# Optimization experiments

Hardware: AMD Instinct MI355X
Metric: run time of the kernel (lower is better)

The kernel has to match this reference:

```python
import jax, jax.numpy as jnp
import numpy as np

HEADS, DIM_HEAD, INNER, DIM = 6, 50, 300, 768
HW, EXTRA, POOL = 100, 150, 10  # spatial side, extra tokens, pool output side
N = HW * HW + EXTRA  # 10150


def setup_inputs() -> dict:
    key = jax.random.key(0)
    ks = jax.random.split(key, 6)
    B = 8
    x = jax.random.normal(ks[0], (B, N, DIM), dtype=jnp.float32)
    # weights scaled ~ typical init so softmax logits are sane
    proj_w = jax.random.normal(ks[1], (INNER, DIM), dtype=jnp.float32) * 0.02
    step_x = jax.random.normal(ks[2], (HEADS, 1, 1), dtype=jnp.float32)
    step_rep = jax.random.normal(ks[3], (HEADS, 1, 1), dtype=jnp.float32)
    out_w = jax.random.normal(ks[4], (DIM, INNER), dtype=jnp.float32) * 0.02
    out_b = jax.random.normal(ks[5], (DIM,), dtype=jnp.float32) * 0.02
    return {"x": x, "proj_w": proj_w, "step_x": step_x, "step_rep": step_rep,
            "out_w": out_w, "out_b": out_b}


def reference(x, proj_w, step_x, step_rep, out_w, out_b):
    b, n, c = x.shape
    hw = int(round((n - EXTRA) ** 0.5))
    scale = DIM_HEAD ** -0.5

    w = x @ proj_w.T  # [b, n, 300]

    # adaptive avg pool of the spatial tokens to (10,10); hw % 10 == 0 -> uniform pooling
    k = hw // POOL
    spatial = w[:, : hw * hw, :].reshape(b, hw, hw, INNER).transpose(0, 3, 1, 2)  # [b,300,hw,hw]
    rep = spatial.reshape(b, INNER, POOL, k, POOL, k).mean(axis=(3, 5))  # [b,300,10,10]
    rep = rep.reshape(b, INNER, POOL * POOL).transpose(0, 2, 1)  # [b,100,300]

    wh = w.reshape(b, n, HEADS, DIM_HEAD).transpose(0, 2, 1, 3)        # [b,h,n,d]
    reph = rep.reshape(b, POOL * POOL, HEADS, DIM_HEAD).transpose(0, 2, 1, 3)  # [b,h,100,d]

    # stage 1: rep attends to all tokens
    dots = jnp.einsum('bhqd,bhkd->bhqk', reph, wh) * scale  # [b,h,100,n]
    attn = jax.nn.softmax(dots, axis=-1)
    rep_delta = jnp.einsum('bhqk,bhkd->bhqd', attn, wh)     # [b,h,100,d]
    reph = reph + step_rep * rep_delta

    # stage 2: rep self-attention, broadcast back through reused attn^T
    dots2 = jnp.einsum('bhqd,bhkd->bhqk', reph, reph) * scale  # [b,h,100,100]
    attn2 = jax.nn.softmax(dots2, axis=-1)
    x_delta = jnp.einsum('bhqk,bhkd->bhqd', attn2, reph)       # [b,h,100,d]
    x_delta = jnp.einsum('bhqn,bhqd->bhnd', attn, x_delta)     # attn^T @ x_delta -> [b,h,n,d]
    x_delta = step_x * x_delta

    x_delta = x_delta.transpose(0, 2, 1, 3).reshape(b, n, HEADS * DIM_HEAD)  # [b,n,300]
    return x_delta @ out_w.T + out_b
```

## Files before the change

kernel.cpp:

```cpp
#include <hip/hip_runtime.h>
#include <math.h>

#define BATCH   8
#define NTOK    10150
#define DIMC    768
#define INNERC  300
#define HEADS   6
#define DHEAD   50
#define NQ      100
#define NBH     48
#define NSPLIT  32
#define CHUNK   320
#define SCALE   0.14142135623730951f
#define MTOT    (BATCH*NTOK)
#define XDK     320
#define NEGBIG  -1.0e30f

typedef __attribute__((ext_vector_type(8))) short short8;
typedef __attribute__((ext_vector_type(4))) float f32x4;

__device__ __forceinline__ ushort f2bf(float x) {
  uint u = __float_as_uint(x);
  uint r = (u + 0x7fffu + ((u >> 16) & 1u)) >> 16;
  return (ushort)r;
}
__device__ __forceinline__ float bf2f(ushort h) {
  return __uint_as_float(((uint)h) << 16);
}

__global__ void split_pad(const float* __restrict__ src, ushort* __restrict__ dHi,
                          ushort* __restrict__ dLo, int R, int C, int Rp, int Cp) {
  const int total = Rp * Cp;
  for (int i = blockIdx.x * blockDim.x + threadIdx.x; i < total;
       i += gridDim.x * blockDim.x) {
    const int r = i / Cp, c = i % Cp;
    const float v = (r < R && c < C) ? src[r * C + c] : 0.f;
    const ushort hh = f2bf(v);
    dHi[i] = hh;
    dLo[i] = f2bf(v - bf2f(hh));
  }
}

__global__ void zero_xd_pad(ushort* __restrict__ xdHi, ushort* __restrict__ xdLo) {
  const int total = MTOT * 20;
  for (int i = blockIdx.x * blockDim.x + threadIdx.x; i < total;
       i += gridDim.x * blockDim.x) {
    const size_t g = (size_t)(i / 20) * XDK + 300 + (i % 20);
    xdHi[g] = 0;
    xdLo[g] = 0;
  }
}

__global__ __launch_bounds__(256, 2) void gemm1_xw(
    const float* __restrict__ x, const ushort* __restrict__ pwHi,
    const ushort* __restrict__ pwLo, ushort* __restrict__ wHi,
    ushort* __restrict__ wLo) {
  __shared__ ushort aH[64][40], aL[64][40];
  __shared__ ushort bH[320][40], bL[320][40];
  const int t = threadIdx.x;
  const int lane = t & 63, wv = t >> 6;
  const int l15 = lane & 15, l4 = lane >> 4;
  const int m0 = blockIdx.x * 64;
  const int arow = t >> 2, aslot = t & 3;

  f32x4 acc[4][5];
#pragma unroll
  for (int i = 0; i < 4; ++i)
#pragma unroll
    for (int j = 0; j < 5; ++j) acc[i][j] = (f32x4){0.f, 0.f, 0.f, 0.f};

  for (int k0 = 0; k0 < DIMC; k0 += 32) {
    __syncthreads();
    {
      float v[8];
      const int m = m0 + arow;
      if (m < MTOT) {
        const float* xp = &x[(size_t)m * DIMC + k0 + aslot * 8];
        const float4 u0 = *(const float4*)xp;
        const float4 u1 = *(const float4*)(xp + 4);
        v[0] = u0.x; v[1] = u0.y; v[2] = u0.z; v[3] = u0.w;
        v[4] = u1.x; v[5] = u1.y; v[6] = u1.z; v[7] = u1.w;
      } else {
#pragma unroll
        for (int j = 0; j < 8; ++j) v[j] = 0.f;
      }
      short8 th, tl;
#pragma unroll
      for (int j = 0; j < 8; ++j) {
        const ushort hh = f2bf(v[j]);
        th[j] = (short)hh;
        tl[j] = (short)f2bf(v[j] - bf2f(hh));
      }
      *(short8*)&aH[arow][aslot * 8] = th;
      *(short8*)&aL[arow][aslot * 8] = tl;
    }
#pragma unroll
    for (int i = 0; i < 5; ++i) {
      const int sid = t + i * 256;
      const int row = sid >> 2, slot = sid & 3;
      const size_t g = (size_t)row * DIMC + k0 + slot * 8;
      *(short8*)&bH[row][slot * 8] = *(const short8*)&pwHi[g];
      *(short8*)&bL[row][slot * 8] = *(const short8*)&pwLo[g];
    }
    __syncthreads();

    short8 ah[4], al[4];
#pragma unroll
    for (int i = 0; i < 4; ++i) {
      ah[i] = *(const short8*)&aH[i * 16 + l15][l4 * 8];
      al[i] = *(const short8*)&aL[i * 16 + l15][l4 * 8];
    }
#pragma unroll
    for (int j = 0; j < 5; ++j) {
      const int brow = wv * 80 + j * 16 + l15;
      const short8 bhf = *(const short8*)&bH[brow][l4 * 8];
      const short8 blf = *(const short8*)&bL[brow][l4 * 8];
#pragma unroll
      for (int i = 0; i < 4; ++i) {
        acc[i][j] = __builtin_amdgcn_mfma_f32_16x16x32_bf16(ah[i], bhf, acc[i][j], 0, 0, 0);
        acc[i][j] = __builtin_amdgcn_mfma_f32_16x16x32_bf16(al[i], bhf, acc[i][j], 0, 0, 0);
        acc[i][j] = __builtin_amdgcn_mfma_f32_16x16x32_bf16(ah[i], blf, acc[i][j], 0, 0, 0);
      }
    }
  }

#pragma unroll
  for (int j = 0; j < 5; ++j) {
    const int col = wv * 80 + j * 16 + l15;
    if (col >= INNERC) continue;
#pragma unroll
    for (int i = 0; i < 4; ++i)
#pragma unroll
      for (int r = 0; r < 4; ++r) {
        const int m = m0 + i * 16 + l4 * 4 + r;
        if (m < MTOT) {
          const float val = acc[i][j][r];
          const ushort hh = f2bf(val);
          const size_t g = (size_t)m * INNERC + col;
          wHi[g] = hh;
          wLo[g] = f2bf(val - bf2f(hh));
        }
      }
  }
}

__global__ __launch_bounds__(256, 2) void gemm2_out(
    const ushort* __restrict__ xdHi, const ushort* __restrict__ xdLo,
    const ushort* __restrict__ owHi, const ushort* __restrict__ owLo,
    const float* __restrict__ out_b, float* __restrict__ out) {
  __shared__ ushort aH[64][40], aL[64][40];
  __shared__ ushort bH[256][40], bL[256][40];
  const int t = threadIdx.x;
  const int lane = t & 63, wv = t >> 6;
  const int l15 = lane & 15, l4 = lane >> 4;
  const int nwg = gridDim.x;
  const int q = nwg >> 3, r = nwg & 7;
  const int xcd = blockIdx.x & 7, idx = blockIdx.x >> 3;
  const int wg = (xcd < r ? xcd * (q + 1) : r * (q + 1) + (xcd - r) * q) + idx;
  const int bn = wg % 3, bm = wg / 3;
  const int m0 = bm * 64, n0 = bn * 256;
  const int arow = t >> 2, aslot = t & 3;

  f32x4 acc[4][4];
#pragma unroll
  for (int i = 0; i < 4; ++i)
#pragma unroll
    for (int j = 0; j < 4; ++j) acc[i][j] = (f32x4){0.f, 0.f, 0.f, 0.f};

  for (int k0 = 0; k0 < XDK; k0 += 32) {
    __syncthreads();
    {
      const int m = m0 + arow;
      if (m < MTOT) {
        const size_t g = (size_t)m * XDK + k0 + aslot * 8;
        *(short8*)&aH[arow][aslot * 8] = *(const short8*)&xdHi[g];
        *(short8*)&aL[arow][aslot * 8] = *(const short8*)&xdLo[g];
      } else {
        const short8 z = {0, 0, 0, 0, 0, 0, 0, 0};
        *(short8*)&aH[arow][aslot * 8] = z;
        *(short8*)&aL[arow][aslot * 8] = z;
      }
    }
#pragma unroll
    for (int i = 0; i < 4; ++i) {
      const int sid = t + i * 256;
      const int row = sid >> 2, slot = sid & 3;
      const size_t g = (size_t)(n0 + row) * XDK + k0 + slot * 8;
      *(short8*)&bH[row][slot * 8] = *(const short8*)&owHi[g];
      *(short8*)&bL[row][slot * 8] = *(const short8*)&owLo[g];
    }
    __syncthreads();

    short8 ah[4], al[4];
#pragma unroll
    for (int i = 0; i < 4; ++i) {
      ah[i] = *(const short8*)&aH[i * 16 + l15][l4 * 8];
      al[i] = *(const short8*)&aL[i * 16 + l15][l4 * 8];
    }
#pragma unroll
    for (int j = 0; j < 4; ++j) {
      const int brow = wv * 64 + j * 16 + l15;
      const short8 bhf = *(const short8*)&bH[brow][l4 * 8];
      const short8 blf = *(const short8*)&bL[brow][l4 * 8];
#pragma unroll
      for (int i = 0; i < 4; ++i) {
        acc[i][j] = __builtin_amdgcn_mfma_f32_16x16x32_bf16(ah[i], bhf, acc[i][j], 0, 0, 0);
        acc[i][j] = __builtin_amdgcn_mfma_f32_16x16x32_bf16(al[i], bhf, acc[i][j], 0, 0, 0);
        acc[i][j] = __builtin_amdgcn_mfma_f32_16x16x32_bf16(ah[i], blf, acc[i][j], 0, 0, 0);
      }
    }
  }

#pragma unroll
  for (int j = 0; j < 4; ++j) {
    const int col = n0 + wv * 64 + j * 16 + l15;
    const float bv = out_b[col];
#pragma unroll
    for (int i = 0; i < 4; ++i)
#pragma unroll
      for (int r = 0; r < 4; ++r) {
        const int m = m0 + i * 16 + l4 * 4 + r;
        if (m < MTOT) out[(size_t)m * DIMC + col] = acc[i][j][r] + bv;
      }
  }
}

__global__ void pool_kernel(const ushort* __restrict__ wHi,
                            const ushort* __restrict__ wLo,
                            float* __restrict__ rep,
                            ushort* __restrict__ repPH, ushort* __restrict__ repPL) {
  int q = blockIdx.x, b = blockIdx.y;
  int i = threadIdx.x;
  if (i < INNERC) {
    int pr = q / 10, pc = q % 10;
    float s = 0.f;
    for (int kr = 0; kr < 10; ++kr)
      for (int kc = 0; kc < 10; ++kc) {
        int tok = (pr * 10 + kr) * 100 + (pc * 10 + kc);
        const size_t g = ((size_t)b * NTOK + tok) * INNERC + i;
        s += bf2f(wHi[g]) + bf2f(wLo[g]);
      }
    s *= 0.01f;
    int h = i / DHEAD, d = i % DHEAD;
    rep[(((size_t)b * HEADS + h) * NQ + q) * DHEAD + d] = s;
    const float sv = s * SCALE;
    const ushort hh = f2bf(sv);
    const size_t pg = (((size_t)b * HEADS + h) * 128 + q) * 64 + d;
    repPH[pg] = hh;
    repPL[pg] = f2bf(sv - bf2f(hh));
  }
  for (int j = threadIdx.x; j < HEADS * 14; j += 320) {
    int h2 = j / 14, d2 = DHEAD + (j % 14);
    const size_t pg = (((size_t)b * HEADS + h2) * 128 + q) * 64 + d2;
    repPH[pg] = 0;
    repPL[pg] = 0;
  }
}

__global__ __launch_bounds__(256, 3) void attn1_mfma(
    const ushort* __restrict__ wHi, const ushort* __restrict__ wLo,
    const float* __restrict__ rep,
    float* __restrict__ m_part, float* __restrict__ l_part,
    float* __restrict__ delta_part) {
  const int bh = blockIdx.x, s = blockIdx.y;
  const int b = bh / HEADS, h = bh % HEADS;
  const int t = threadIdx.x;
  const int lane = t & 63, wv = t >> 6;
  const int l15 = lane & 15, l4 = lane >> 4;

  __shared__ ushort Khi[32][72], Klo[32][72];
  __shared__ ushort VThi[64][40], VTlo[64][40];
  __shared__ ushort Phi[128][40], Plo[128][40];

  short8 qhi[2][2], qlo[2][2];
#pragma unroll
  for (int mi = 0; mi < 2; ++mi) {
#pragma unroll
    for (int ks = 0; ks < 2; ++ks) {
      const int qr = 32 * wv + 16 * mi + l15;
      short8 th, tl;
#pragma unroll
      for (int j = 0; j < 8; ++j) {
        const int k = 32 * ks + 8 * l4 + j;
        float v = (qr < NQ && k < DHEAD)
                      ? rep[((size_t)bh * NQ + qr) * DHEAD + k] * SCALE : 0.f;
        ushort hh = f2bf(v);
        th[j] = (short)hh;
        tl[j] = (short)f2bf(v - bf2f(hh));
      }
      qhi[mi][ks] = th; qlo[mi][ks] = tl;
    }
  }

  f32x4 accO[2][4];
  float m_run[2][4], l_run[2][4];
#pragma unroll
  for (int mi = 0; mi < 2; ++mi) {
#pragma unroll
    for (int r = 0; r < 4; ++r) { m_run[mi][r] = NEGBIG; l_run[mi][r] = 0.f; }
#pragma unroll
    for (int di = 0; di < 4; ++di) accO[mi][di] = (f32x4){0.f, 0.f, 0.f, 0.f};
  }

  const int n0 = s * CHUNK;
  const int n1 = min(NTOK, n0 + CHUNK);

  for (int nt = n0; nt < n1; nt += 32) {
    __syncthreads();
#pragma unroll
    for (int i = 0; i < 4; ++i) {
      const int idx = t + i * 256;
      const int tr = idx >> 5;
      const int d = (idx & 31) * 2;
      const bool inb = (nt + tr < n1) && (d < DHEAD);
      uint hv = 0, lv = 0;
      if (inb) {
        const size_t g = ((size_t)b * NTOK + nt + tr) * INNERC + h * DHEAD + d;
        hv = *(const uint*)&wHi[g];
        lv = *(const uint*)&wLo[g];
      }
      *(uint*)&Khi[tr][d] = hv;
      *(uint*)&Klo[tr][d] = lv;
      const int ps = ((((tr >> 3) + (d >> 3)) & 3) << 3) + (tr & 7);
      VThi[d][ps] = (ushort)(hv & 0xffffu);
      VTlo[d][ps] = (ushort)(lv & 0xffffu);
      VThi[d + 1][ps] = (ushort)(hv >> 16);
      VTlo[d + 1][ps] = (ushort)(lv >> 16);
    }
    __syncthreads();

    f32x4 accS[2][2];
#pragma unroll
    for (int mi = 0; mi < 2; ++mi)
#pragma unroll
      for (int ni = 0; ni < 2; ++ni) accS[mi][ni] = (f32x4){0.f, 0.f, 0.f, 0.f};
#pragma unroll
    for (int ks = 0; ks < 2; ++ks) {
      short8 kh[2], kl[2];
#pragma unroll
      for (int ni = 0; ni < 2; ++ni) {
        kh[ni] = *(const short8*)&Khi[16 * ni + l15][32 * ks + 8 * l4];
        kl[ni] = *(const short8*)&Klo[16 * ni + l15][32 * ks + 8 * l4];
      }
#pragma unroll
      for (int mi = 0; mi < 2; ++mi)
#pragma unroll
        for (int ni = 0; ni < 2; ++ni) {
          accS[mi][ni] = __builtin_amdgcn_mfma_f32_16x16x32_bf16(qhi[mi][ks], kh[ni], accS[mi][ni], 0, 0, 0);
          accS[mi][ni] = __builtin_amdgcn_mfma_f32_16x16x32_bf16(qlo[mi][ks], kh[ni], accS[mi][ni], 0, 0, 0);
          accS[mi][ni] = __builtin_amdgcn_mfma_f32_16x16x32_bf16(qhi[mi][ks], kl[ni], accS[mi][ni], 0, 0, 0);
        }
    }

    bool cval[2];
#pragma unroll
    for (int ni = 0; ni < 2; ++ni) cval[ni] = (nt + 16 * ni + l15) < n1;
#pragma unroll
    for (int mi = 0; mi < 2; ++mi) {
#pragma unroll
      for (int ni = 0; ni < 2; ++ni)
        if (!cval[ni]) {
#pragma unroll
          for (int r = 0; r < 4; ++r) accS[mi][ni][r] = NEGBIG;
        }
#pragma unroll
      for (int r = 0; r < 4; ++r) {
        float mx = fmaxf(accS[mi][0][r], accS[mi][1][r]);
        mx = fmaxf(mx, __shfl_xor(mx, 1));
        mx = fmaxf(mx, __shfl_xor(mx, 2));
        mx = fmaxf(mx, __shfl_xor(mx, 4));
        mx = fmaxf(mx, __shfl_xor(mx, 8));
        const float m_new = fmaxf(m_run[mi][r], mx);
        const float sc = __expf(m_run[mi][r] - m_new);
        m_run[mi][r] = m_new;
        l_run[mi][r] *= sc;
#pragma unroll
        for (int di = 0; di < 4; ++di) accO[mi][di][r] *= sc;
        float ps = 0.f;
#pragma unroll
        for (int ni = 0; ni < 2; ++ni) {
          const float p = __expf(accS[mi][ni][r] - m_new);
          accS[mi][ni][r] = p;
          ps += p;
        }
        ps += __shfl_xor(ps, 1);
        ps += __shfl_xor(ps, 2);
        ps += __shfl_xor(ps, 4);
        ps += __shfl_xor(ps, 8);
        l_run[mi][r] += ps;
      }
#pragma unroll
      for (int ni = 0; ni < 2; ++ni)
#pragma unroll
        for (int r = 0; r < 4; ++r) {
          const int row = 32 * wv + 16 * mi + 4 * l4 + r;
          const int col = 16 * ni + l15;
          const float p = accS[mi][ni][r];
          const ushort ph = f2bf(p);
          Phi[row][col] = ph;
          Plo[row][col] = f2bf(p - bf2f(ph));
        }
    }

#pragma unroll
    for (int mi = 0; mi < 2; ++mi) {
      const short8 pah = *(const short8*)&Phi[32 * wv + 16 * mi + l15][8 * l4];
      const short8 pal = *(const short8*)&Plo[32 * wv + 16 * mi + l15][8 * l4];
#pragma unroll
      for (int di = 0; di < 4; ++di) {
        const int vs = (((l4 + 2 * di + (l15 >> 3)) & 3)) << 3;
        const short8 vbh = *(const short8*)&VThi[16 * di + l15][vs];
        const short8 vbl = *(const short8*)&VTlo[16 * di + l15][vs];
        accO[mi][di] = __builtin_amdgcn_mfma_f32_16x16x32_bf16(pah, vbh, accO[mi][di], 0, 0, 0);
        accO[mi][di] = __builtin_amdgcn_mfma_f32_16x16x32_bf16(pal, vbh, accO[mi][di], 0, 0, 0);
        accO[mi][di] = __builtin_amdgcn_mfma_f32_16x16x32_bf16(pah, vbl, accO[mi][di], 0, 0, 0);
      }
    }
  }

  const size_t base = ((size_t)bh * NSPLIT + s) * NQ;
#pragma unroll
  for (int mi = 0; mi < 2; ++mi)
#pragma unroll
    for (int r = 0; r < 4; ++r) {
      const int q = 32 * wv + 16 * mi + 4 * l4 + r;
      if (q < NQ && l15 == 0) {
        m_part[base + q] = m_run[mi][r];
        l_part[base + q] = l_run[mi][r];
      }
#pragma unroll
      for (int di = 0; di < 4; ++di) {
        const int d = 16 * di + l15;
        if (q < NQ && d < DHEAD)
          delta_part[(base + q) * DHEAD + d] = accO[mi][di][r];
      }
    }
}

__global__ __launch_bounds__(256) void attn1_combine(
    const float* __restrict__ rep, const float* __restrict__ m_part,
    const float* __restrict__ l_part, const float* __restrict__ delta_part,
    const float* __restrict__ step_rep,
    float* __restrict__ reph2, float* __restrict__ m_fin, float* __restrict__ l_fin) {
  int bh = blockIdx.x;
  int h = bh % HEADS;
  int t = threadIdx.x;
  __shared__ float Mf[NQ], Lf[NQ];
  if (t < NQ) {
    int q = t;
    float M = -INFINITY;
#pragma unroll
    for (int s2 = 0; s2 < NSPLIT; ++s2)
      M = fmaxf(M, m_part[((size_t)bh * NSPLIT + s2) * NQ + q]);
    float L = 0.f;
#pragma unroll
    for (int s2 = 0; s2 < NSPLIT; ++s2)
      L += l_part[((size_t)bh * NSPLIT + s2) * NQ + q] *
           __expf(m_part[((size_t)bh * NSPLIT + s2) * NQ + q] - M);
    Mf[q] = M; Lf[q] = L;
    m_fin[(size_t)bh * NQ + q] = M;
    l_fin[(size_t)bh * NQ + q] = L;
  }
  __syncthreads();
  float sr = step_rep[h];
  for (int idx = t; idx < NQ * DHEAD; idx += 256) {
    int q = idx / DHEAD, d = idx % DHEAD;
    float sum = 0.f;
#pragma unroll
    for (int s2 = 0; s2 < NSPLIT; ++s2) {
      size_t pb = ((size_t)bh * NSPLIT + s2) * NQ + q;
      sum += __expf(m_part[pb] - Mf[q]) * delta_part[pb * DHEAD + d];
    }
    float rd = sum / Lf[q];
    reph2[(size_t)bh * NQ * DHEAD + idx] =
        rep[(size_t)bh * NQ * DHEAD + idx] + sr * rd;
  }
}

__global__ __launch_bounds__(256) void attn2_kernel(
    const float* __restrict__ reph2, const float* __restrict__ step_x,
    ushort* __restrict__ xqTH, ushort* __restrict__ xqTL) {
  int bh = blockIdx.x;
  int h = bh % HEADS;
  int t = threadIdx.x;
  __shared__ float r2[NQ * DHEAD];
  __shared__ float att[NQ * NQ];

  for (int idx = t; idx < NQ * DHEAD; idx += 256)
    r2[idx] = reph2[(size_t)bh * NQ * DHEAD + idx];
  __syncthreads();

  for (int idx = t; idx < NQ * NQ; idx += 256) {
    int qq = idx / NQ, jj = idx % NQ;
    float s = 0.f;
#pragma unroll
    for (int k = 0; k < DHEAD; ++k) s += r2[qq * DHEAD + k] * r2[jj * DHEAD + k];
    att[idx] = s * SCALE;
  }
  __syncthreads();
  if (t < NQ) {
    float M = -INFINITY;
    for (int j = 0; j < NQ; ++j) M = fmaxf(M, att[t * NQ + j]);
    float L = 0.f;
    for (int j = 0; j < NQ; ++j) { float e = __expf(att[t * NQ + j] - M); att[t * NQ + j] = e; L += e; }
    float inv = 1.f / L;
    for (int j = 0; j < NQ; ++j) att[t * NQ + j] *= inv;
  }
  __syncthreads();
  float sx = step_x[h];
  for (int idx = t; idx < NQ * DHEAD; idx += 256) {
    int qd_q = idx / DHEAD, d = idx % DHEAD;
    float v = 0.f;
#pragma unroll
    for (int j = 0; j < NQ; ++j) v += att[qd_q * NQ + j] * r2[j * DHEAD + d];
    v *= sx;
    const size_t pg = ((size_t)bh * 64 + d) * 128 + qd_q;
    const ushort hh = f2bf(v);
    xqTH[pg] = hh;
    xqTL[pg] = f2bf(v - bf2f(hh));
  }
  for (int idx = t; idx < 64 * 28; idx += 256) {
    int d = idx / 28, qq2 = NQ + (idx % 28);
    const size_t pg = ((size_t)bh * 64 + d) * 128 + qq2;
    xqTH[pg] = 0;
    xqTL[pg] = 0;
  }
}

#define TT5 128
__global__ __launch_bounds__(256, 2) void bcast5_kernel(
    const ushort* __restrict__ wHi, const ushort* __restrict__ wLo,
    const ushort* __restrict__ repPH, const ushort* __restrict__ repPL,
    const ushort* __restrict__ xqTH, const ushort* __restrict__ xqTL,
    const float* __restrict__ m_fin, const float* __restrict__ l_fin,
    ushort* __restrict__ xdHi, ushort* __restrict__ xdLo) {
  const int tile = blockIdx.x, bh = blockIdx.y;
  const int b = bh / HEADS, h = bh % HEADS;
  const int tok0 = tile * TT5;
  const int t = threadIdx.x;
  const int lane = t & 63, wv = t >> 6;
  const int l15 = lane & 15, l4 = lane >> 4;

  __shared__ ushort pH[128][72], pL[128][72];

  short8 awh[2][2], awl[2][2];
#pragma unroll
  for (int st = 0; st < 2; ++st) {
    const int tokA = tok0 + st * 64 + 16 * wv + l15;
#pragma unroll
    for (int ks = 0; ks < 2; ++ks) {
      const int kbase = 32 * ks + 8 * l4;
      uint hv[4] = {0, 0, 0, 0}, lv[4] = {0, 0, 0, 0};
      if (tokA < NTOK && kbase < DHEAD) {
        const size_t g = ((size_t)b * NTOK + tokA) * INNERC + h * DHEAD + kbase;
#pragma unroll
        for (int c = 0; c < 4; ++c) {
          hv[c] = *(const uint*)&wHi[g + 2 * c];
          lv[c] = *(const uint*)&wLo[g + 2 * c];
        }
      }
      short8 th, tl;
#pragma unroll
      for (int j = 0; j < 8; ++j) {
        const bool ok = (kbase + j) < DHEAD;
        const ushort hsel = (j & 1) ? (ushort)(hv[j >> 1] >> 16) : (ushort)(hv[j >> 1] & 0xffffu);
        const ushort lsel = (j & 1) ? (ushort)(lv[j >> 1] >> 16) : (ushort)(lv[j >> 1] & 0xffffu);
        th[j] = ok ? (short)hsel : (short)0;
        tl[j] = ok ? (short)lsel : (short)0;
      }
      awh[st][ks] = th;
      awl[st][ks] = tl;
    }
  }

  f32x4 accO[2][4];
#pragma unroll
  for (int st = 0; st < 2; ++st)
#pragma unroll
    for (int di = 0; di < 4; ++di) accO[st][di] = (f32x4){0.f, 0.f, 0.f, 0.f};

#pragma unroll
  for (int qc = 0; qc < 2; ++qc) {
    const int q0 = qc * 64;

    short8 rbh[4][2], rbl[4][2];
#pragma unroll
    for (int ni = 0; ni < 4; ++ni)
#pragma unroll
      for (int ks = 0; ks < 2; ++ks) {
        const size_t rg = (((size_t)bh * 128) + (q0 + 16 * ni + l15)) * 64 + 32 * ks + 8 * l4;
        rbh[ni][ks] = *(const short8*)&repPH[rg];
        rbl[ni][ks] = *(const short8*)&repPL[rg];
      }
    float mq[4], li[4];
    bool vq[4];
#pragma unroll
    for (int ni = 0; ni < 4; ++ni) {
      const int q = q0 + 16 * ni + l15;
      vq[ni] = (q < NQ);
      mq[ni] = vq[ni] ? m_fin[(size_t)bh * NQ + q] : 0.f;
      li[ni] = vq[ni] ? 1.f / l_fin[(size_t)bh * NQ + q] : 0.f;
    }

#pragma unroll
    for (int st = 0; st < 2; ++st) {
      f32x4 accS[4];
#pragma unroll
      for (int ni = 0; ni < 4; ++ni) accS[ni] = (f32x4){0.f, 0.f, 0.f, 0.f};
#pragma unroll
      for (int ks = 0; ks < 2; ++ks)
#pragma unroll
        for (int ni = 0; ni < 4; ++ni) {
          accS[ni] = __builtin_amdgcn_mfma_f32_16x16x32_bf16(awh[st][ks], rbh[ni][ks], accS[ni], 0, 0, 0);
          accS[ni] = __builtin_amdgcn_mfma_f32_16x16x32_bf16(awl[st][ks], rbh[ni][ks], accS[ni], 0, 0, 0);
          accS[ni] = __builtin_amdgcn_mfma_f32_16x16x32_bf16(awh[st][ks], rbl[ni][ks], accS[ni], 0, 0, 0);
        }
#pragma unroll
      for (int ni = 0; ni < 4; ++ni) {
#pragma unroll
        for (int r = 0; r < 4; ++r) {
          const float p = vq[ni] ? __expf(accS[ni][r] - mq[ni]) * li[ni] : 0.f;
          const int row = st * 64 + 16 * wv + 4 * l4 + r;
          const ushort ph = f2bf(p);
          pH[row][16 * ni + l15] = ph;
          pL[row][16 * ni + l15] = f2bf(p - bf2f(ph));
        }
      }
    }

    short8 xbh[4][2], xbl[4][2];
#pragma unroll
    for (int di = 0; di < 4; ++di)
#pragma unroll
      for (int ks2 = 0; ks2 < 2; ++ks2) {
        const size_t xg = (((size_t)bh * 64) + (16 * di + l15)) * 128 + q0 + 32 * ks2 + 8 * l4;
        xbh[di][ks2] = *(const short8*)&xqTH[xg];
        xbl[di][ks2] = *(const short8*)&xqTL[xg];
      }

#pragma unroll
    for (int st = 0; st < 2; ++st) {
#pragma unroll
      for (int ks2 = 0; ks2 < 2; ++ks2) {
        const short8 pah = *(const short8*)&pH[st * 64 + 16 * wv + l15][32 * ks2 + 8 * l4];
        const short8 pal = *(const short8*)&pL[st * 64 + 16 * wv + l15][32 * ks2 + 8 * l4];
#pragma unroll
        for (int di = 0; di < 4; ++di) {
          accO[st][di] = __builtin_amdgcn_mfma_f32_16x16x32_bf16(pah, xbh[di][ks2], accO[st][di], 0, 0, 0);
          accO[st][di] = __builtin_amdgcn_mfma_f32_16x16x32_bf16(pal, xbh[di][ks2], accO[st][di], 0, 0, 0);
          accO[st][di] = __builtin_amdgcn_mfma_f32_16x16x32_bf16(pah, xbl[di][ks2], accO[st][di], 0, 0, 0);
        }
      }
    }
  }

#pragma unroll
  for (int st = 0; st < 2; ++st)
#pragma unroll
    for (int di = 0; di < 4; ++di) {
      const int d = di * 16 + l15;
      if (d >= DHEAD) continue;
#pragma unroll
      for (int r = 0; r < 4; ++r) {
        const int tok = tok0 + st * 64 + wv * 16 + 4 * l4 + r;
        if (tok < NTOK) {
          const float val = accO[st][di][r];
          const ushort hh = f2bf(val);
          const size_t g = ((size_t)b * NTOK + tok) * XDK + h * DHEAD + d;
          xdHi[g] = hh;
          xdLo[g] = f2bf(val - bf2f(hh));
        }
      }
    }
}

extern "C" void kernel_launch(void* const* d_in, const int* in_sizes, int n_in,
                              void* d_out, int out_size, void* d_ws, size_t ws_size,
                              hipStream_t stream) {
  const float* x        = (const float*)d_in[0];
  const float* proj_w   = (const float*)d_in[1];
  const float* step_x   = (const float*)d_in[2];
  const float* step_rep = (const float*)d_in[3];
  const float* out_w    = (const float*)d_in[4];
  const float* out_b    = (const float*)d_in[5];
  float* out = (float*)d_out;

  uint8_t* p8 = (uint8_t*)d_ws;
  ushort* wHi    = (ushort*)(p8);
  ushort* wLo    = (ushort*)(p8 + 48720000);
  float*  rep    = (float*) (p8 + 97440000);
  float*  reph2  = (float*) (p8 + 98400000);
  float*  m_part = (float*) (p8 + 100320000);
  float*  l_part = (float*) (p8 + 100934400);
  float*  m_fin  = (float*) (p8 + 101548800);
  float*  l_fin  = (float*) (p8 + 101568000);
  ushort* xdHi   = (ushort*)(p8 + 101587200);
  ushort* xdLo   = (ushort*)(p8 + 153555200);
  ushort* pwHi   = (ushort*)(p8 + 205523200);
  ushort* pwLo   = (ushort*)(p8 + 206014720);
  ushort* owHi   = (ushort*)(p8 + 206506240);
  ushort* owLo   = (ushort*)(p8 + 206997760);
  ushort* repPH  = (ushort*)(p8 + 207489280);
  ushort* repPL  = (ushort*)(p8 + 208275712);
  ushort* xqTH   = (ushort*)(p8 + 209062144);
  ushort* xqTL   = (ushort*)(p8 + 209848576);
  float* delta = (float*)xdHi;

  split_pad<<<960, 256, 0, stream>>>(proj_w, pwHi, pwLo, INNERC, DIMC, 320, DIMC);
  split_pad<<<960, 256, 0, stream>>>(out_w, owHi, owLo, DIMC, INNERC, DIMC, XDK);
  gemm1_xw<<<1269, 256, 0, stream>>>(x, pwHi, pwLo, wHi, wLo);
  pool_kernel<<<dim3(NQ, BATCH), 320, 0, stream>>>(wHi, wLo, rep, repPH, repPL);
  attn1_mfma<<<dim3(NBH, NSPLIT), 256, 0, stream>>>(wHi, wLo, rep, m_part, l_part, delta);
  attn1_combine<<<NBH, 256, 0, stream>>>(rep, m_part, l_part, delta, step_rep,
                                         reph2, m_fin, l_fin);
  zero_xd_pad<<<2048, 256, 0, stream>>>(xdHi, xdLo);
  attn2_kernel<<<NBH, 256, 0, stream>>>(reph2, step_x, xqTH, xqTL);
  bcast5_kernel<<<dim3(80, NBH), 256, 0, stream>>>(
      wHi, wLo, repPH, repPL, xqTH, xqTL, m_fin, l_fin, xdHi, xdLo);
  gemm2_out<<<3807, 256, 0, stream>>>(xdHi, xdLo, owHi, owLo, out_b, out);
}
```

Before: 758.9 us.

## Use 128-row tiles with 8-wave workgroups in both split-bf16 GEMMs

Both projection GEMMs move from 64-row tiles run by 4 waves to 128-row tiles run by 8 waves arranged 2x4. Each staged weight tile in LDS is now reused by twice as many rows, which roughly halves the weight traffic per output row and halves the workgroup count. The LDS row stride also changes from 40 to 44 to alter the bank-conflict pattern. The tighter launch bounds (512 threads, 4 blocks) may force the compiler into a small VGPR budget, which risks register spills. The larger LDS footprint also limits how many workgroups fit on a CU.

New measurement: 816.1 us. 7.5% more time.

```diff
diff --git a/kernel.cpp b/kernel.cpp
--- a/kernel.cpp
+++ b/kernel.cpp
@@ -15,6 +15,7 @@
 #define MTOT    (BATCH*NTOK)
 #define XDK     320
 #define NEGBIG  -1.0e30f
+#define LDS_S   44
 
 typedef __attribute__((ext_vector_type(8))) short short8;
 typedef __attribute__((ext_vector_type(4))) float f32x4;
@@ -51,16 +52,17 @@
   }
 }
 
-__global__ __launch_bounds__(256, 2) void gemm1_xw(
+__global__ __launch_bounds__(512, 4) void gemm1_xw(
     const float* __restrict__ x, const ushort* __restrict__ pwHi,
     const ushort* __restrict__ pwLo, ushort* __restrict__ wHi,
     ushort* __restrict__ wLo) {
-  __shared__ ushort aH[64][40], aL[64][40];
-  __shared__ ushort bH[320][40], bL[320][40];
+  __shared__ ushort aH[128][LDS_S], aL[128][LDS_S];
+  __shared__ ushort bH[320][LDS_S], bL[320][LDS_S];
   const int t = threadIdx.x;
-  const int lane = t & 63, wv = t >> 6;
+  const int lane = t & 63, w = t >> 6;
+  const int wr = w >> 2, wc = w & 3;
   const int l15 = lane & 15, l4 = lane >> 4;
-  const int m0 = blockIdx.x * 64;
+  const int m0 = blockIdx.x * 128;
   const int arow = t >> 2, aslot = t & 3;
 
   f32x4 acc[4][5];
@@ -95,24 +97,27 @@
       *(short8*)&aL[arow][aslot * 8] = tl;
     }
 #pragma unroll
-    for (int i = 0; i < 5; ++i) {
-      const int sid = t + i * 256;
-      const int row = sid >> 2, slot = sid & 3;
-      const size_t g = (size_t)row * DIMC + k0 + slot * 8;
-      *(short8*)&bH[row][slot * 8] = *(const short8*)&pwHi[g];
-      *(short8*)&bL[row][slot * 8] = *(const short8*)&pwLo[g];
+    for (int i = 0; i < 3; ++i) {
+      const int sid = t + i * 512;
+      if (sid < 1280) {
+        const int row = sid >> 2, slot = sid & 3;
+        const size_t g = (size_t)row * DIMC + k0 + slot * 8;
+        *(short8*)&bH[row][slot * 8] = *(const short8*)&pwHi[g];
+        *(short8*)&bL[row][slot * 8] = *(const short8*)&pwLo[g];
+      }
     }
     __syncthreads();
 
     short8 ah[4], al[4];
 #pragma unroll
     for (int i = 0; i < 4; ++i) {
-      ah[i] = *(const short8*)&aH[i * 16 + l15][l4 * 8];
-      al[i] = *(const short8*)&aL[i * 16 + l15][l4 * 8];
+      const int row = wr * 64 + i * 16 + l15;
+      ah[i] = *(const short8*)&aH[row][l4 * 8];
+      al[i] = *(const short8*)&aL[row][l4 * 8];
     }
 #pragma unroll
     for (int j = 0; j < 5; ++j) {
-      const int brow = wv * 80 + j * 16 + l15;
+      const int brow = wc * 80 + j * 16 + l15;
       const short8 bhf = *(const short8*)&bH[brow][l4 * 8];
       const short8 blf = *(const short8*)&bL[brow][l4 * 8];
 #pragma unroll
@@ -126,13 +131,13 @@
 
 #pragma unroll
   for (int j = 0; j < 5; ++j) {
-    const int col = wv * 80 + j * 16 + l15;
+    const int col = wc * 80 + j * 16 + l15;
     if (col >= INNERC) continue;
 #pragma unroll
     for (int i = 0; i < 4; ++i)
 #pragma unroll
       for (int r = 0; r < 4; ++r) {
-        const int m = m0 + i * 16 + l4 * 4 + r;
+        const int m = m0 + wr * 64 + i * 16 + l4 * 4 + r;
         if (m < MTOT) {
           const float val = acc[i][j][r];
           const ushort hh = f2bf(val);
@@ -144,21 +149,22 @@
   }
 }
 
-__global__ __launch_bounds__(256, 2) void gemm2_out(
+__global__ __launch_bounds__(512, 4) void gemm2_out(
     const ushort* __restrict__ xdHi, const ushort* __restrict__ xdLo,
     const ushort* __restrict__ owHi, const ushort* __restrict__ owLo,
     const float* __restrict__ out_b, float* __restrict__ out) {
-  __shared__ ushort aH[64][40], aL[64][40];
-  __shared__ ushort bH[256][40], bL[256][40];
+  __shared__ ushort aH[128][LDS_S], aL[128][LDS_S];
+  __shared__ ushort bH[256][LDS_S], bL[256][LDS_S];
   const int t = threadIdx.x;
-  const int lane = t & 63, wv = t >> 6;
+  const int lane = t & 63, w = t >> 6;
+  const int wr = w >> 2, wc = w & 3;
   const int l15 = lane & 15, l4 = lane >> 4;
   const int nwg = gridDim.x;
   const int q = nwg >> 3, r = nwg & 7;
   const int xcd = blockIdx.x & 7, idx = blockIdx.x >> 3;
   const int wg = (xcd < r ? xcd * (q + 1) : r * (q + 1) + (xcd - r) * q) + idx;
   const int bn = wg % 3, bm = wg / 3;
-  const int m0 = bm * 64, n0 = bn * 256;
+  const int m0 = bm * 128, n0 = bn * 256;
   const int arow = t >> 2, aslot = t & 3;
 
   f32x4 acc[4][4];
@@ -182,8 +188,8 @@
       }
     }
 #pragma unroll
-    for (int i = 0; i < 4; ++i) {
-      const int sid = t + i * 256;
+    for (int i = 0; i < 2; ++i) {
+      const int sid = t + i * 512;
       const int row = sid >> 2, slot = sid & 3;
       const size_t g = (size_t)(n0 + row) * XDK + k0 + slot * 8;
       *(short8*)&bH[row][slot * 8] = *(const short8*)&owHi[g];
@@ -194,12 +200,13 @@
     short8 ah[4], al[4];
 #pragma unroll
     for (int i = 0; i < 4; ++i) {
-      ah[i] = *(const short8*)&aH[i * 16 + l15][l4 * 8];
-      al[i] = *(const short8*)&aL[i * 16 + l15][l4 * 8];
+      const int row = wr * 64 + i * 16 + l15;
+      ah[i] = *(const short8*)&aH[row][l4 * 8];
+      al[i] = *(const short8*)&aL[row][l4 * 8];
     }
 #pragma unroll
     for (int j = 0; j < 4; ++j) {
-      const int brow = wv * 64 + j * 16 + l15;
+      const int brow = wc * 64 + j * 16 + l15;
       const short8 bhf = *(const short8*)&bH[brow][l4 * 8];
       const short8 blf = *(const short8*)&bL[brow][l4 * 8];
 #pragma unroll
@@ -213,13 +220,13 @@
 
 #pragma unroll
   for (int j = 0; j < 4; ++j) {
-    const int col = n0 + wv * 64 + j * 16 + l15;
+    const int col = n0 + wc * 64 + j * 16 + l15;
     const float bv = out_b[col];
 #pragma unroll
     for (int i = 0; i < 4; ++i)
 #pragma unroll
       for (int r = 0; r < 4; ++r) {
-        const int m = m0 + i * 16 + l4 * 4 + r;
+        const int m = m0 + wr * 64 + i * 16 + l4 * 4 + r;
         if (m < MTOT) out[(size_t)m * DIMC + col] = acc[i][j][r] + bv;
       }
   }
@@ -708,7 +715,7 @@
 
   split_pad<<<960, 256, 0, stream>>>(proj_w, pwHi, pwLo, INNERC, DIMC, 320, DIMC);
   split_pad<<<960, 256, 0, stream>>>(out_w, owHi, owLo, DIMC, INNERC, DIMC, XDK);
-  gemm1_xw<<<1269, 256, 0, stream>>>(x, pwHi, pwLo, wHi, wLo);
+  gemm1_xw<<<635, 512, 0, stream>>>(x, pwHi, pwLo, wHi, wLo);
   pool_kernel<<<dim3(NQ, BATCH), 320, 0, stream>>>(wHi, wLo, rep, repPH, repPL);
   attn1_mfma<<<dim3(NBH, NSPLIT), 256, 0, stream>>>(wHi, wLo, rep, m_part, l_part, delta);
   attn1_combine<<<NBH, 256, 0, stream>>>(rep, m_part, l_part, delta, step_rep,
@@ -717,5 +724,5 @@
   attn2_kernel<<<NBH, 256, 0, stream>>>(reph2, step_x, xqTH, xqTL);
   bcast5_kernel<<<dim3(80, NBH), 256, 0, stream>>>(
       wHi, wLo, repPH, repPL, xqTH, xqTL, m_fin, l_fin, xdHi, xdLo);
-  gemm2_out<<<3807, 256, 0, stream>>>(xdHi, xdLo, owHi, owLo, out_b, out);
-}
+  gemm2_out<<<1905, 512, 0, stream>>>(xdHi, xdLo, owHi, owLo, out_b, out);
+}
```
